# Optimization experiments

Hardware: AMD Instinct MI355X
Metric: run time of the kernel (lower is better)

## Reference

```python
import jax, jax.numpy as jnp
import numpy as np

DIM = 1024
DIM_HEAD = 64
HEADS = 16
BATCH = 2
SEQ = 2048
SCALE = DIM_HEAD ** -0.5


def setup_inputs() -> dict:
    key = jax.random.key(0)
    ks = jax.random.split(key, 5)
    tokens = jax.random.normal(ks[0], (BATCH, SEQ, DIM), dtype=jnp.float32)
    wq = jax.random.normal(ks[1], (HEADS, DIM, DIM_HEAD), dtype=jnp.float32)
    wk = jax.random.normal(ks[2], (HEADS, DIM, DIM_HEAD), dtype=jnp.float32)
    wv = jax.random.normal(ks[3], (HEADS, DIM, DIM_HEAD), dtype=jnp.float32)
    wo = jax.random.normal(ks[4], (HEADS, DIM_HEAD, DIM), dtype=jnp.float32)
    return {"tokens": tokens, "wq": wq, "wk": wk, "wv": wv, "wo": wo}


def reference(tokens, wq, wk, wv, wo):
    # q, k, v: [b, h, n, dh]
    q = jnp.einsum('bnd,hde->bhne', tokens, wq) * SCALE
    k = jnp.einsum('bnd,hde->bhne', tokens, wk)
    v = jnp.einsum('bnd,hde->bhne', tokens, wv)
    sim = jnp.einsum('bhie,bhje->bhij', q, k)          # [b, h, n, n]
    attn = jax.nn.softmax(sim, axis=-1)
    aggregated = jnp.einsum('bhij,bhje->bhie', attn, v)  # [b, h, n, dh]
    retrieved = jnp.einsum('bhne,hed->bnd', aggregated, wo)  # sum over heads
    return retrieved
```

## Files before the change

### kernel.cpp

```cpp
#include <hip/hip_runtime.h>
#include <hip/hip_fp16.h>
#include <stdint.h>

#define BB 2
#define HH 16
#define SS 2048
#define DD 1024
#define DHH 64
#define QSCALE 0.18033688011112042f

typedef _Float16 half8 __attribute__((ext_vector_type(8)));
typedef _Float16 half4 __attribute__((ext_vector_type(4)));
typedef __fp16 fp16x2 __attribute__((ext_vector_type(2)));
typedef float floatx4 __attribute__((ext_vector_type(4)));

__device__ __forceinline__ floatx4 mfma16(half8 a, half8 b, floatx4 c) {
  return __builtin_amdgcn_mfma_f32_16x16x32_f16(a, b, c, 0, 0, 0);
}

__device__ __forceinline__ void dma16(const _Float16* g, _Float16* l) {
  __builtin_amdgcn_global_load_lds(
      (const __attribute__((address_space(1))) uint32_t*)g,
      (__attribute__((address_space(3))) uint32_t*)l,
      16, 0, 0);
}

#define DRAIN_BARRIER() do { \
  asm volatile("s_waitcnt vmcnt(0) lgkmcnt(0)" ::: "memory"); \
  __syncthreads(); \
} while (0)


__global__ __launch_bounds__(256) void convert_kernel(
    const float* __restrict__ wq, const float* __restrict__ wk,
    const float* __restrict__ wv, const float* __restrict__ wo,
    _Float16* __restrict__ Wh, _Float16* __restrict__ Wl,
    _Float16* __restrict__ Wot)
{
  __shared__ float St[64][68];
  const int kt = blockIdx.x;
  const int hy = blockIdx.y;
  const int z  = blockIdx.z;
  const int t  = (int)threadIdx.x;
  const int k0 = kt * 64;

  const float* src = (z == 0) ? (wq + hy * (DD * DHH))
                   : (z == 1) ? (wk + hy * (DD * DHH))
                   : (z == 2) ? (wv + hy * (DD * DHH))
                   : wo;

  const int rr = t >> 4, cc = (t & 15) * 4;
  if (z < 3) {
    #pragma unroll
    for (int i = 0; i < 4; ++i)
      *(floatx4*)&St[rr + 16 * i][cc] =
          *(const floatx4*)(src + (k0 + rr + 16 * i) * DHH + cc);
  } else {
    const int d0 = hy * 64;
    #pragma unroll
    for (int i = 0; i < 4; ++i)
      *(floatx4*)&St[rr + 16 * i][cc] =
          *(const floatx4*)(src + (k0 + rr + 16 * i) * 1024 + d0 + cc);
  }
  __syncthreads();

  const int e = t >> 2, kc = (t & 3) * 16;
  if (z < 3) {
    const int n = z * 1024 + hy * 64 + e;
    half8 hi0, hi1, lo0, lo1;
    #pragma unroll
    for (int u = 0; u < 16; ++u) {
      float x = St[kc + u][e];
      _Float16 hh = (_Float16)x;
      _Float16 ll = (_Float16)(x - (float)hh);
      if (u < 8) { hi0[u] = hh; lo0[u] = ll; }
      else       { hi1[u - 8] = hh; lo1[u - 8] = ll; }
    }
    *(half8*)(Wh + n * 1024 + k0 + kc)     = hi0;
    *(half8*)(Wh + n * 1024 + k0 + kc + 8) = hi1;
    *(half8*)(Wl + n * 1024 + k0 + kc)     = lo0;
    *(half8*)(Wl + n * 1024 + k0 + kc + 8) = lo1;
  } else {
    const int d0 = hy * 64;
    half8 hi0, hi1;
    #pragma unroll
    for (int u = 0; u < 16; ++u) {
      _Float16 hh = (_Float16)St[kc + u][e];
      if (u < 8) hi0[u] = hh; else hi1[u - 8] = hh;
    }
    *(half8*)(Wot + (d0 + e) * 1024 + k0 + kc)     = hi0;
    *(half8*)(Wot + (d0 + e) * 1024 + k0 + kc + 8) = hi1;
  }
}

__global__ __launch_bounds__(256) void tokens_split_kernel(
    const float* __restrict__ tokens,
    _Float16* __restrict__ th, _Float16* __restrict__ tl)
{
  const int i = ((int)blockIdx.x * 256 + (int)threadIdx.x) * 8;
  floatx4 x0 = *(const floatx4*)(tokens + i);
  floatx4 x1 = *(const floatx4*)(tokens + i + 4);
  half8 h, l;
  #pragma unroll
  for (int j = 0; j < 8; ++j) {
    float x = (j < 4) ? x0[j] : x1[j - 4];
    _Float16 hh = (_Float16)x;
    h[j] = hh;
    l[j] = (_Float16)(x - (float)hh);
  }
  *(half8*)(th + i) = h;
  *(half8*)(tl + i) = l;
}

__global__ __launch_bounds__(256) void qkv_gemm_kernel(
    const _Float16* __restrict__ th, const _Float16* __restrict__ tl,
    const _Float16* __restrict__ Wh, const _Float16* __restrict__ Wl,
    _Float16* __restrict__ qh, _Float16* __restrict__ ql,
    _Float16* __restrict__ kh, _Float16* __restrict__ kl,
    _Float16* __restrict__ vt)
{
  __shared__ alignas(16) _Float16 sbuf[2][4][128 * 32];

  const int n0 = blockIdx.x * 128;
  const int m0 = blockIdx.y * 128;
  const int zb = n0 >> 10;
  const bool is_v = (zb == 2);
  const int t = (int)threadIdx.x;
  const int lane = t & 63, wid = t >> 6;
  const int l16 = lane & 15, q4 = lane >> 4;
  const int mw = (wid & 1) * 64, nw = (wid >> 1) * 64;

  const int g  = (lane & 7) ^ ((lane >> 3) & 7);
  const int grow  = (lane >> 3) * 2 + (g >> 2);
  const int gcol8 = (g & 3) * 8;
  const int laneoff = (l16 >> 1) * 128 + (((((l16 & 1) << 2) | q4) ^ (l16 >> 1)) * 16);

  const _Float16* src;
  int arr;
  if (wid == 0)      { src = th + m0 * 1024; arr = 0; }
  else if (wid == 1) { src = Wh + n0 * 1024; arr = 1; }
  else if (wid == 2) { src = Wl + n0 * 1024; arr = 2; }
  else               { src = tl + m0 * 1024; arr = 3; }
  const bool stage_active = !(is_v && wid == 3);
  const _Float16* gsrc = src + grow * 1024 + gcol8;

  const floatx4 z4 = {0.0f, 0.0f, 0.0f, 0.0f};
  floatx4 acc[4][4];
  #pragma unroll
  for (int mi = 0; mi < 4; ++mi)
    #pragma unroll
    for (int ni = 0; ni < 4; ++ni) acc[mi][ni] = z4;

  auto stage = [&](int buf, int kt2) {
    if (stage_active) {
      const _Float16* gp = gsrc + kt2 * 32;
      _Float16* dst = &sbuf[buf][arr][0];
      #pragma unroll
      for (int j = 0; j < 8; ++j)
        dma16(gp + j * 16 * 1024, dst + j * 16 * 32);
    }
  };

  auto compute = [&](int buf) {
    const char* sAh = (const char*)&sbuf[buf][0][0];
    const char* sBh = (const char*)&sbuf[buf][1][0];
    const char* sBl = (const char*)&sbuf[buf][2][0];
    const char* sAl = (const char*)&sbuf[buf][3][0];
    half8 a_h[4];
    #pragma unroll
    for (int mi = 0; mi < 4; ++mi)
      a_h[mi] = *(const half8*)(sAh + (mw + mi * 16) * 64 + laneoff);
    if (!is_v) {
      half8 a_l[4];
      #pragma unroll
      for (int mi = 0; mi < 4; ++mi)
        a_l[mi] = *(const half8*)(sAl + (mw + mi * 16) * 64 + laneoff);
      #pragma unroll
      for (int ni = 0; ni < 4; ++ni) {
        const half8 b_h = *(const half8*)(sBh + (nw + ni * 16) * 64 + laneoff);
        const half8 b_l = *(const half8*)(sBl + (nw + ni * 16) * 64 + laneoff);
        #pragma unroll
        for (int mi = 0; mi < 4; ++mi) {
          acc[mi][ni] = mfma16(a_h[mi], b_h, acc[mi][ni]);
          acc[mi][ni] = mfma16(a_h[mi], b_l, acc[mi][ni]);
          acc[mi][ni] = mfma16(a_l[mi], b_h, acc[mi][ni]);
        }
      }
    } else {
      #pragma unroll
      for (int ni = 0; ni < 4; ++ni) {
        const half8 b_h = *(const half8*)(sBh + (nw + ni * 16) * 64 + laneoff);
        const half8 b_l = *(const half8*)(sBl + (nw + ni * 16) * 64 + laneoff);
        #pragma unroll
        for (int mi = 0; mi < 4; ++mi) {
          acc[mi][ni] = mfma16(a_h[mi], b_h, acc[mi][ni]);
          acc[mi][ni] = mfma16(a_h[mi], b_l, acc[mi][ni]);
        }
      }
    }
  };

  stage(0, 0);
  DRAIN_BARRIER();

  #pragma unroll 1
  for (int kt = 0; kt < 32; kt += 2) {
    if (kt + 1 < 32) stage(1, kt + 1);
    compute(0);
    DRAIN_BARRIER();
    if (kt + 2 < 32) stage(0, kt + 2);
    compute(1);
    DRAIN_BARRIER();
  }

  #pragma unroll
  for (int ni = 0; ni < 4; ++ni) {
    const int ncol = n0 + nw + ni * 16;
    const int h = (ncol >> 6) & 15;
    const int e = (ncol & 63) + l16;
    #pragma unroll
    for (int mi = 0; mi < 4; ++mi) {
      #pragma unroll
      for (int r = 0; r < 4; ++r) {
        const int grow2 = m0 + mw + mi * 16 + q4 * 4 + r;
        const int b = grow2 >> 11, s = grow2 & 2047;
        const float v = acc[mi][ni][r];
        const int qkidx = ((b * HH + h) * SS + s) * DHH + e;
        if (zb == 0) {
          const float vs = v * QSCALE;
          const _Float16 hh = (_Float16)vs;
          qh[qkidx] = hh;
          ql[qkidx] = (_Float16)(vs - (float)hh);
        } else if (zb == 1) {
          const _Float16 hh = (_Float16)v;
          kh[qkidx] = hh;
          kl[qkidx] = (_Float16)(v - (float)hh);
        } else {
          vt[((b * HH + h) * DHH + e) * SS + s] = (_Float16)v;
        }
      }
    }
  }
}

__global__ __launch_bounds__(512) void attn_kernel(
    const _Float16* __restrict__ qh, const _Float16* __restrict__ ql,
    const _Float16* __restrict__ kh, const _Float16* __restrict__ kl,
    const _Float16* __restrict__ vt, _Float16* __restrict__ agg)
{
  __shared__ _Float16 Kh[64][72], Kl[64][72], Vs[64][72];
  __shared__ _Float16 Ps[128][72];

  const int qt = blockIdx.x;
  const int h  = blockIdx.y;
  const int b  = blockIdx.z;
  const int bh = b * HH + h;
  const int t = (int)threadIdx.x;
  const int lane = t & 63, wid = t >> 6;
  const int l16 = lane & 15, q4 = lane >> 4;

  const int sr = t >> 3, sc = (t & 7) * 8;

  half8 qfh[2], qfl[2];
  {
    const int s = qt * 128 + wid * 16 + l16;
    const int base = (bh * SS + s) * DHH + q4 * 8;
    qfh[0] = *(const half8*)(qh + base);
    qfh[1] = *(const half8*)(qh + base + 32);
    qfl[0] = *(const half8*)(ql + base);
    qfl[1] = *(const half8*)(ql + base + 32);
  }

  const floatx4 z4 = {0.0f, 0.0f, 0.0f, 0.0f};
  floatx4 o[4], osum;
  #pragma unroll
  for (int i = 0; i < 4; ++i) o[i] = z4;
  osum = z4;
  float m_r = -1e30f;

  const half8 ones = {1.f16, 1.f16, 1.f16, 1.f16, 1.f16, 1.f16, 1.f16, 1.f16};

  half8 pK, pL, pV;
  {
    const int gk = (bh * SS + sr) * DHH + sc;
    pK = *(const half8*)(kh + gk);
    pL = *(const half8*)(kl + gk);
    pV = *(const half8*)(vt + (bh * DHH + sr) * SS + sc);
  }

  for (int kt = 0; kt < 32; ++kt) {
    __syncthreads();
    *(half8*)&Kh[sr][sc] = pK;
    *(half8*)&Kl[sr][sc] = pL;
    *(half8*)&Vs[sr][sc] = pV;
    __syncthreads();

    if (kt < 31) {
      const int k1 = (kt + 1) * 64;
      const int gk = (bh * SS + k1 + sr) * DHH + sc;
      pK = *(const half8*)(kh + gk);
      pL = *(const half8*)(kl + gk);
      pV = *(const half8*)(vt + (bh * DHH + sr) * SS + k1 + sc);
    }

    floatx4 sv[4];
    #pragma unroll
    for (int sub = 0; sub < 4; ++sub) {
      const half8 ah0 = *(const half8*)&Kh[sub * 16 + l16][q4 * 8];
      const half8 ah1 = *(const half8*)&Kh[sub * 16 + l16][q4 * 8 + 32];
      const half8 al0 = *(const half8*)&Kl[sub * 16 + l16][q4 * 8];
      const half8 al1 = *(const half8*)&Kl[sub * 16 + l16][q4 * 8 + 32];
      floatx4 s4 = z4;
      s4 = mfma16(ah0, qfh[0], s4);
      s4 = mfma16(ah1, qfh[1], s4);
      s4 = mfma16(al0, qfh[0], s4);
      s4 = mfma16(al1, qfh[1], s4);
      s4 = mfma16(ah0, qfl[0], s4);
      s4 = mfma16(ah1, qfl[1], s4);
      sv[sub] = s4;
    }

    float mx = fmaxf(fmaxf(sv[0][0], sv[0][1]), fmaxf(sv[0][2], sv[0][3]));
    #pragma unroll
    for (int sub = 1; sub < 4; ++sub)
      mx = fmaxf(mx, fmaxf(fmaxf(sv[sub][0], sv[sub][1]),
                           fmaxf(sv[sub][2], sv[sub][3])));
    mx = fmaxf(mx, __shfl_xor(mx, 16));
    mx = fmaxf(mx, __shfl_xor(mx, 32));
    const float mnew = fmaxf(m_r, mx);

    #pragma unroll
    for (int sub = 0; sub < 4; ++sub)
      #pragma unroll
      for (int r = 0; r < 4; ++r)
        sv[sub][r] = exp2f(sv[sub][r] - mnew);

    #pragma unroll
    for (int sub = 0; sub < 4; ++sub) {
      fp16x2 p01 = __builtin_amdgcn_cvt_pkrtz(sv[sub][0], sv[sub][1]);
      fp16x2 p23 = __builtin_amdgcn_cvt_pkrtz(sv[sub][2], sv[sub][3]);
      half4 pv;
      pv[0] = (_Float16)p01[0]; pv[1] = (_Float16)p01[1];
      pv[2] = (_Float16)p23[0]; pv[3] = (_Float16)p23[1];
      *(half4*)&Ps[wid * 16 + l16][sub * 16 + q4 * 4] = pv;
    }

    if (__any(mnew > m_r)) {
      const float alpha = exp2f(m_r - mnew);
      m_r = mnew;
      #pragma unroll
      for (int sub = 0; sub < 4; ++sub)
        #pragma unroll
        for (int r = 0; r < 4; ++r) o[sub][r] *= alpha;
      #pragma unroll
      for (int r = 0; r < 4; ++r) osum[r] *= alpha;
    }

    asm volatile("s_waitcnt lgkmcnt(0)" ::: "memory");

    const half8 pb0 = *(const half8*)&Ps[wid * 16 + l16][q4 * 8];
    const half8 pb1 = *(const half8*)&Ps[wid * 16 + l16][q4 * 8 + 32];
    #pragma unroll
    for (int sub = 0; sub < 4; ++sub) {
      const half8 va0 = *(const half8*)&Vs[sub * 16 + l16][q4 * 8];
      const half8 va1 = *(const half8*)&Vs[sub * 16 + l16][q4 * 8 + 32];
      o[sub] = mfma16(va0, pb0, o[sub]);
      o[sub] = mfma16(va1, pb1, o[sub]);
    }
    osum = mfma16(ones, pb0, osum);
    osum = mfma16(ones, pb1, osum);
  }

  const float inv = 1.0f / osum[0];
  const int s = qt * 128 + wid * 16 + l16;
  #pragma unroll
  for (int sub = 0; sub < 4; ++sub) {
    half4 ov;
    #pragma unroll
    for (int r = 0; r < 4; ++r) ov[r] = (_Float16)(o[sub][r] * inv);
    *(half4*)(agg + (b * SS + s) * (HH * DHH) + h * DHH + sub * 16 + q4 * 4) = ov;
  }
}

__global__ __launch_bounds__(256) void out_gemm_kernel(
    const _Float16* __restrict__ agg, const _Float16* __restrict__ Wot,
    float* __restrict__ out)
{
  __shared__ alignas(16) _Float16 sbuf[2][2][128 * 32];
  const int n0 = blockIdx.x * 128;
  const int m0 = blockIdx.y * 128;
  const int t = (int)threadIdx.x;
  const int lane = t & 63, wid = t >> 6;
  const int l16 = lane & 15, q4 = lane >> 4;
  const int mw = (wid & 1) * 64, nw = (wid >> 1) * 64;

  const int g  = (lane & 7) ^ ((lane >> 3) & 7);
  const int grow  = (lane >> 3) * 2 + (g >> 2);
  const int gcol8 = (g & 3) * 8;
  const int laneoff = (l16 >> 1) * 128 + (((((l16 & 1) << 2) | q4) ^ (l16 >> 1)) * 16);

  const int arr = wid >> 1;
  const int half64 = (wid & 1) * 64;
  const _Float16* src = (arr == 0) ? (agg + m0 * 1024) : (Wot + n0 * 1024);
  const _Float16* gsrc = src + (half64 + grow) * 1024 + gcol8;

  const floatx4 z4 = {0.0f, 0.0f, 0.0f, 0.0f};
  floatx4 acc[4][4];
  #pragma unroll
  for (int mi = 0; mi < 4; ++mi)
    #pragma unroll
    for (int ni = 0; ni < 4; ++ni) acc[mi][ni] = z4;

  auto stage = [&](int buf, int kt2) {
    const _Float16* gp = gsrc + kt2 * 32;
    _Float16* dst = &sbuf[buf][arr][half64 * 32];
    #pragma unroll
    for (int j = 0; j < 4; ++j)
      dma16(gp + j * 16 * 1024, dst + j * 16 * 32);
  };

  auto compute = [&](int buf) {
    const char* sA = (const char*)&sbuf[buf][0][0];
    const char* sB = (const char*)&sbuf[buf][1][0];
    half8 a_f[4];
    #pragma unroll
    for (int mi = 0; mi < 4; ++mi)
      a_f[mi] = *(const half8*)(sA + (mw + mi * 16) * 64 + laneoff);
    #pragma unroll
    for (int ni = 0; ni < 4; ++ni) {
      const half8 b_f = *(const half8*)(sB + (nw + ni * 16) * 64 + laneoff);
      #pragma unroll
      for (int mi = 0; mi < 4; ++mi)
        acc[mi][ni] = mfma16(a_f[mi], b_f, acc[mi][ni]);
    }
  };

  stage(0, 0);
  DRAIN_BARRIER();

  #pragma unroll 1
  for (int kt = 0; kt < 32; kt += 2) {
    if (kt + 1 < 32) stage(1, kt + 1);
    compute(0);
    DRAIN_BARRIER();
    if (kt + 2 < 32) stage(0, kt + 2);
    compute(1);
    DRAIN_BARRIER();
  }

  #pragma unroll
  for (int ni = 0; ni < 4; ++ni)
    #pragma unroll
    for (int mi = 0; mi < 4; ++mi)
      #pragma unroll
      for (int r = 0; r < 4; ++r)
        out[(m0 + mw + mi * 16 + q4 * 4 + r) * 1024 + n0 + nw + ni * 16 + l16] =
            acc[mi][ni][r];
}

extern "C" void kernel_launch(void* const* d_in, const int* in_sizes, int n_in,
                              void* d_out, int out_size, void* d_ws, size_t ws_size,
                              hipStream_t stream)
{
  const float* tokens = (const float*)d_in[0];
  const float* wq = (const float*)d_in[1];
  const float* wk = (const float*)d_in[2];
  const float* wv = (const float*)d_in[3];
  const float* wo = (const float*)d_in[4];
  float* out = (float*)d_out;

  char* ws = (char*)d_ws;
  _Float16* qh  = (_Float16*)(ws);
  _Float16* ql  = (_Float16*)(ws + 8388608);
  _Float16* kh  = (_Float16*)(ws + 16777216);
  _Float16* kl  = (_Float16*)(ws + 25165824);
  _Float16* vt  = (_Float16*)(ws + 33554432);
  _Float16* Wh  = (_Float16*)(ws + 41943040);
  _Float16* Wl  = (_Float16*)(ws + 48234496);
  _Float16* Wot = (_Float16*)(ws + 54525952);
  _Float16* th  = (_Float16*)(ws + 56623104);
  _Float16* tl  = (_Float16*)(ws + 65011712);
  _Float16* agg = (_Float16*)(ws + 56623104);

  convert_kernel<<<dim3(16, 16, 4), 256, 0, stream>>>(wq, wk, wv, wo, Wh, Wl, Wot);
  tokens_split_kernel<<<2048, 256, 0, stream>>>(tokens, th, tl);
  qkv_gemm_kernel<<<dim3(24, 32), 256, 0, stream>>>(th, tl, Wh, Wl, qh, ql, kh, kl, vt);
  attn_kernel<<<dim3(16, 16, 2), 512, 0, stream>>>(qh, ql, kh, kl, vt, agg);
  out_gemm_kernel<<<dim3(8, 32), 256, 0, stream>>>(agg, Wot, out);
}
```

Baseline: 285.7 us.

## Double attention key tile to 128 and fold running max into MFMA bias

Each loop iteration of the flash-attention kernel now processes 128 keys instead of 64, halving the number of iterations and barrier pairs, with K/V tiles and register prefetch doubled. The running max is subtracted by seeding the QK accumulator with -m_r, so the exponent no longer needs a per-element subtraction except when the max grows. The max starts at 0 rather than -inf. More registers and LDS are used per block, which may reduce occupancy. The P buffer is reused for the two 64-key halves within an iteration.

```diff
diff --git a/kernel.cpp b/kernel.cpp
--- a/kernel.cpp
+++ b/kernel.cpp
@@ -248,7 +248,8 @@
     const _Float16* __restrict__ kh, const _Float16* __restrict__ kl,
     const _Float16* __restrict__ vt, _Float16* __restrict__ agg)
 {
-  __shared__ _Float16 Kh[64][72], Kl[64][72], Vs[64][72];
+  __shared__ _Float16 Kh[128][72], Kl[128][72];
+  __shared__ _Float16 Vs[64][136];
   __shared__ _Float16 Ps[128][72];
 
   const int qt = blockIdx.x;
@@ -259,7 +260,8 @@
   const int lane = t & 63, wid = t >> 6;
   const int l16 = lane & 15, q4 = lane >> 4;
 
-  const int sr = t >> 3, sc = (t & 7) * 8;
+  const int srK = t >> 3, scK = (t & 7) * 8;
+  const int srV = t >> 4, scV = (t & 15) * 8;
 
   half8 qfh[2], qfl[2];
   {
@@ -276,41 +278,53 @@
   #pragma unroll
   for (int i = 0; i < 4; ++i) o[i] = z4;
   osum = z4;
-  float m_r = -1e30f;
+  float m_r = 0.0f;
 
   const half8 ones = {1.f16, 1.f16, 1.f16, 1.f16, 1.f16, 1.f16, 1.f16, 1.f16};
 
-  half8 pK, pL, pV;
+  half8 pK0, pK1, pL0, pL1, pV0, pV1;
   {
-    const int gk = (bh * SS + sr) * DHH + sc;
-    pK = *(const half8*)(kh + gk);
-    pL = *(const half8*)(kl + gk);
-    pV = *(const half8*)(vt + (bh * DHH + sr) * SS + sc);
-  }
-
-  for (int kt = 0; kt < 32; ++kt) {
+    const int gk = (bh * SS + srK) * DHH + scK;
+    pK0 = *(const half8*)(kh + gk);
+    pK1 = *(const half8*)(kh + gk + 64 * DHH);
+    pL0 = *(const half8*)(kl + gk);
+    pL1 = *(const half8*)(kl + gk + 64 * DHH);
+    const int gv = (bh * DHH + srV) * SS + scV;
+    pV0 = *(const half8*)(vt + gv);
+    pV1 = *(const half8*)(vt + gv + 32 * SS);
+  }
+
+  for (int kt = 0; kt < 16; ++kt) {
     __syncthreads();
-    *(half8*)&Kh[sr][sc] = pK;
-    *(half8*)&Kl[sr][sc] = pL;
-    *(half8*)&Vs[sr][sc] = pV;
+    *(half8*)&Kh[srK][scK]      = pK0;
+    *(half8*)&Kh[64 + srK][scK] = pK1;
+    *(half8*)&Kl[srK][scK]      = pL0;
+    *(half8*)&Kl[64 + srK][scK] = pL1;
+    *(half8*)&Vs[srV][scV]      = pV0;
+    *(half8*)&Vs[32 + srV][scV] = pV1;
     __syncthreads();
 
-    if (kt < 31) {
-      const int k1 = (kt + 1) * 64;
-      const int gk = (bh * SS + k1 + sr) * DHH + sc;
-      pK = *(const half8*)(kh + gk);
-      pL = *(const half8*)(kl + gk);
-      pV = *(const half8*)(vt + (bh * DHH + sr) * SS + k1 + sc);
-    }
-
-    floatx4 sv[4];
-    #pragma unroll
-    for (int sub = 0; sub < 4; ++sub) {
+    if (kt < 15) {
+      const int k1 = (kt + 1) * 128;
+      const int gk = (bh * SS + k1 + srK) * DHH + scK;
+      pK0 = *(const half8*)(kh + gk);
+      pK1 = *(const half8*)(kh + gk + 64 * DHH);
+      pL0 = *(const half8*)(kl + gk);
+      pL1 = *(const half8*)(kl + gk + 64 * DHH);
+      const int gv = (bh * DHH + srV) * SS + k1 + scV;
+      pV0 = *(const half8*)(vt + gv);
+      pV1 = *(const half8*)(vt + gv + 32 * SS);
+    }
+
+    floatx4 sv[8];
+    const floatx4 bias = {-m_r, -m_r, -m_r, -m_r};
+    #pragma unroll
+    for (int sub = 0; sub < 8; ++sub) {
       const half8 ah0 = *(const half8*)&Kh[sub * 16 + l16][q4 * 8];
       const half8 ah1 = *(const half8*)&Kh[sub * 16 + l16][q4 * 8 + 32];
       const half8 al0 = *(const half8*)&Kl[sub * 16 + l16][q4 * 8];
       const half8 al1 = *(const half8*)&Kl[sub * 16 + l16][q4 * 8 + 32];
-      floatx4 s4 = z4;
+      floatx4 s4 = bias;
       s4 = mfma16(ah0, qfh[0], s4);
       s4 = mfma16(ah1, qfh[1], s4);
       s4 = mfma16(al0, qfh[0], s4);
@@ -322,32 +336,20 @@
 
     float mx = fmaxf(fmaxf(sv[0][0], sv[0][1]), fmaxf(sv[0][2], sv[0][3]));
     #pragma unroll
-    for (int sub = 1; sub < 4; ++sub)
+    for (int sub = 1; sub < 8; ++sub)
       mx = fmaxf(mx, fmaxf(fmaxf(sv[sub][0], sv[sub][1]),
                            fmaxf(sv[sub][2], sv[sub][3])));
     mx = fmaxf(mx, __shfl_xor(mx, 16));
     mx = fmaxf(mx, __shfl_xor(mx, 32));
-    const float mnew = fmaxf(m_r, mx);
-
-    #pragma unroll
-    for (int sub = 0; sub < 4; ++sub)
-      #pragma unroll
-      for (int r = 0; r < 4; ++r)
-        sv[sub][r] = exp2f(sv[sub][r] - mnew);
-
-    #pragma unroll
-    for (int sub = 0; sub < 4; ++sub) {
-      fp16x2 p01 = __builtin_amdgcn_cvt_pkrtz(sv[sub][0], sv[sub][1]);
-      fp16x2 p23 = __builtin_amdgcn_cvt_pkrtz(sv[sub][2], sv[sub][3]);
-      half4 pv;
-      pv[0] = (_Float16)p01[0]; pv[1] = (_Float16)p01[1];
-      pv[2] = (_Float16)p23[0]; pv[3] = (_Float16)p23[1];
-      *(half4*)&Ps[wid * 16 + l16][sub * 16 + q4 * 4] = pv;
-    }
-
-    if (__any(mnew > m_r)) {
-      const float alpha = exp2f(m_r - mnew);
-      m_r = mnew;
+
+    if (__any(mx > 0.0f)) {
+      const float shift = fmaxf(mx, 0.0f);
+      const float alpha = exp2f(-shift);
+      m_r += shift;
+      #pragma unroll
+      for (int sub = 0; sub < 8; ++sub)
+        #pragma unroll
+        for (int r = 0; r < 4; ++r) sv[sub][r] -= shift;
       #pragma unroll
       for (int sub = 0; sub < 4; ++sub)
         #pragma unroll
@@ -355,20 +357,37 @@
       #pragma unroll
       for (int r = 0; r < 4; ++r) osum[r] *= alpha;
     }
-
-    asm volatile("s_waitcnt lgkmcnt(0)" ::: "memory");
-
-    const half8 pb0 = *(const half8*)&Ps[wid * 16 + l16][q4 * 8];
-    const half8 pb1 = *(const half8*)&Ps[wid * 16 + l16][q4 * 8 + 32];
-    #pragma unroll
-    for (int sub = 0; sub < 4; ++sub) {
-      const half8 va0 = *(const half8*)&Vs[sub * 16 + l16][q4 * 8];
-      const half8 va1 = *(const half8*)&Vs[sub * 16 + l16][q4 * 8 + 32];
-      o[sub] = mfma16(va0, pb0, o[sub]);
-      o[sub] = mfma16(va1, pb1, o[sub]);
-    }
-    osum = mfma16(ones, pb0, osum);
-    osum = mfma16(ones, pb1, osum);
+    #pragma unroll
+    for (int sub = 0; sub < 8; ++sub)
+      #pragma unroll
+      for (int r = 0; r < 4; ++r)
+        sv[sub][r] = exp2f(sv[sub][r]);
+
+    #pragma unroll
+    for (int half = 0; half < 2; ++half) {
+      #pragma unroll
+      for (int sub = 0; sub < 4; ++sub) {
+        const floatx4 s4 = sv[half * 4 + sub];
+        fp16x2 p01 = __builtin_amdgcn_cvt_pkrtz(s4[0], s4[1]);
+        fp16x2 p23 = __builtin_amdgcn_cvt_pkrtz(s4[2], s4[3]);
+        half4 pv;
+        pv[0] = (_Float16)p01[0]; pv[1] = (_Float16)p01[1];
+        pv[2] = (_Float16)p23[0]; pv[3] = (_Float16)p23[1];
+        *(half4*)&Ps[wid * 16 + l16][sub * 16 + q4 * 4] = pv;
+      }
+      asm volatile("s_waitcnt lgkmcnt(0)" ::: "memory");
+      const half8 pb0 = *(const half8*)&Ps[wid * 16 + l16][q4 * 8];
+      const half8 pb1 = *(const half8*)&Ps[wid * 16 + l16][q4 * 8 + 32];
+      #pragma unroll
+      for (int sub = 0; sub < 4; ++sub) {
+        const half8 va0 = *(const half8*)&Vs[sub * 16 + l16][half * 64 + q4 * 8];
+        const half8 va1 = *(const half8*)&Vs[sub * 16 + l16][half * 64 + q4 * 8 + 32];
+        o[sub] = mfma16(va0, pb0, o[sub]);
+        o[sub] = mfma16(va1, pb1, o[sub]);
+      }
+      osum = mfma16(ones, pb0, osum);
+      osum = mfma16(ones, pb1, osum);
+    }
   }
 
   const float inv = 1.0f / osum[0];
```

After: 273.0 us. -4.5%, faster.
